# Kernel tuning notes

Measured on AMD Instinct MI355X. Metric: run time of the kernel, lower is better.

## Reference

```python
import jax, jax.numpy as jnp
import numpy as np

L = 4          # num layers
NH = 128       # hidden channels per layer
FC = 16        # frame_channel = patch^2 * C
HP = 32        # H / patch
WP = 32        # W / patch
K = 5          # filter_size
B = 8
T_PREV = 10
T_AFTER = 10
T_TOTAL = T_PREV + T_AFTER - 1  # 19 generated frames
FORGET_BIAS = 1.0


def _conv(x, w):
    # x: [B, Cin, H, W], w: [Cout, Cin, kh, kw], stride 1, SAME padding
    return jax.lax.conv_general_dilated(
        x, w, (1, 1), 'SAME', dimension_numbers=('NCHW', 'OIHW', 'NCHW'))


def _st_lstm_cell(x, h, c, m, Wx, Wh, Wm, Wo, Wl):
    # Standard PredRNN SpatioTemporalLSTMCell (bias-free convs, no layer norm)
    xc = _conv(x, Wx)   # [B, 7*NH, H, W]
    hc = _conv(h, Wh)   # [B, 4*NH, H, W]
    mc = _conv(m, Wm)   # [B, 3*NH, H, W]
    i_x, f_x, g_x, i_xp, f_xp, g_xp, o_x = jnp.split(xc, 7, axis=1)
    i_h, f_h, g_h, o_h = jnp.split(hc, 4, axis=1)
    i_m, f_m, g_m = jnp.split(mc, 3, axis=1)

    i_t = jax.nn.sigmoid(i_x + i_h)
    f_t = jax.nn.sigmoid(f_x + f_h + FORGET_BIAS)
    g_t = jnp.tanh(g_x + g_h)
    c_new = f_t * c + i_t * g_t

    i_tp = jax.nn.sigmoid(i_xp + i_m)
    f_tp = jax.nn.sigmoid(f_xp + f_m + FORGET_BIAS)
    g_tp = jnp.tanh(g_xp + g_m)
    m_new = f_tp * m + i_tp * g_tp

    mem = jnp.concatenate([c_new, m_new], axis=1)  # [B, 2*NH, H, W]
    o_t = jax.nn.sigmoid(o_x + o_h + _conv(mem, Wo))
    h_new = o_t * jnp.tanh(_conv(mem, Wl))
    return h_new, c_new, m_new


def setup_inputs() -> dict:
    key = jax.random.key(0)
    ks = jax.random.split(key, 9)
    s = jnp.float32(0.02)  # small init scale to keep gates in a sane range
    return {
        'frames_tensor': jax.random.normal(ks[0], (B, T_PREV + T_AFTER, HP, WP, FC), jnp.float32),
        'mask_true': jax.random.uniform(ks[1], (B, T_AFTER - 1, HP, WP, FC), jnp.float32),
        'Wx0': jax.random.normal(ks[2], (7 * NH, FC, K, K), jnp.float32) * s,
        'Wx': jax.random.normal(ks[3], (L - 1, 7 * NH, NH, K, K), jnp.float32) * s,
        'Wh': jax.random.normal(ks[4], (L, 4 * NH, NH, K, K), jnp.float32) * s,
        'Wm': jax.random.normal(ks[5], (L, 3 * NH, NH, K, K), jnp.float32) * s,
        'Wo': jax.random.normal(ks[6], (L, NH, 2 * NH, K, K), jnp.float32) * s,
        'Wl': jax.random.normal(ks[7], (L, NH, 2 * NH, 1, 1), jnp.float32) * s,
        'Wout': jax.random.normal(ks[8], (FC, NH, 1, 1), jnp.float32) * s,
    }


def reference(frames_tensor, mask_true, Wx0, Wx, Wh, Wm, Wo, Wl, Wout):
    # [B,T,H,W,C] -> [B,T,C,H,W]
    frames = jnp.transpose(frames_tensor, (0, 1, 4, 2, 3))
    mask = jnp.transpose(mask_true, (0, 1, 4, 2, 3))

    # For t < data_previous the input is the ground-truth frame (mask == 1);
    # afterwards it is blended with the previous generation x_gen.
    ones = jnp.ones((B, T_PREV, FC, HP, WP), frames.dtype)
    mask_seq = jnp.concatenate([ones, mask], axis=1)  # [B, T_TOTAL, C, H, W]

    frames_t = jnp.transpose(frames[:, :T_TOTAL], (1, 0, 2, 3, 4))  # [T,B,C,H,W]
    mask_t = jnp.transpose(mask_seq, (1, 0, 2, 3, 4))               # [T,B,C,H,W]

    h0 = jnp.zeros((L, B, NH, HP, WP), frames.dtype)
    c0 = jnp.zeros((L, B, NH, HP, WP), frames.dtype)
    m0 = jnp.zeros((B, NH, HP, WP), frames.dtype)
    xg0 = jnp.zeros((B, FC, HP, WP), frames.dtype)

    def step(carry, xs):
        h, c, m, x_gen = carry
        frame, msk = xs
        net = msk * frame + (1.0 - msk) * x_gen
        h_new, c_new, m = _st_lstm_cell(net, h[0], c[0], m, Wx0, Wh[0], Wm[0], Wo[0], Wl[0])
        hs, cs = [h_new], [c_new]
        for i in range(1, L):
            hi, ci, m = _st_lstm_cell(hs[-1], h[i], c[i], m, Wx[i - 1], Wh[i], Wm[i], Wo[i], Wl[i])
            hs.append(hi)
            cs.append(ci)
        x_gen = _conv(hs[-1], Wout)  # 1x1 conv, no bias
        return (jnp.stack(hs), jnp.stack(cs), m, x_gen), x_gen

    _, next_frames = jax.lax.scan(step, (h0, c0, m0, xg0), (frames_t, mask_t))
    # [T,B,C,H,W] -> [B,T,H,W,C]
    return jnp.transpose(next_frames, (1, 0, 3, 4, 2))
```

## Files before the change

kernel.cpp:

```cpp
#include <hip/hip_runtime.h>
#include <math.h>

#define TT 19
#define TPREV 10

typedef __attribute__((ext_vector_type(8))) short bf8v;
typedef __attribute__((ext_vector_type(4))) float f4v;
typedef __attribute__((ext_vector_type(16))) float f16v;

__device__ __forceinline__ float sigmoidf_(float x){ return 1.f/(1.f+expf(-x)); }
__device__ __forceinline__ unsigned short f2bf(float x){
    unsigned int u = __float_as_uint(x);
    u += 0x7FFFu + ((u>>16)&1u);
    return (unsigned short)(u>>16);
}
__device__ __forceinline__ float bf2f(unsigned short b){ return __uint_as_float(((unsigned int)b)<<16); }

#define GLDS(g, l) __builtin_amdgcn_global_load_lds( \
    (const __attribute__((address_space(1))) void*)(g),   \
    (__attribute__((address_space(3))) void*)(l), 16, 0, 0)

struct HSeg {
    const unsigned short* in;
    int cl;
    int c0;
    int nch;
    int tap0, ntaps, five;
};
struct HJob {
    const unsigned short* wt;
    float* out;
    int cout_stride, pad;
    HSeg s;
};
struct HJobs14 { HJob j[14]; };
struct HJobs9  { HJob j[9]; };

__device__ __forceinline__ void stage_halo(
    unsigned short* sH, const unsigned short* inb, int cl, int c0,
    int y0, int tid)
{
#pragma unroll
    for (int k = 0; k < 8; ++k) {
        const int s = tid + k * 256;
        if (s < 1920) {
            const int r = s / 160;
            const int rem = s - r * 160;
            const int cc = rem >> 2, G = rem & 3;
            const int y = y0 + r - 2, x = cc - 4;
            const bool okv = ((unsigned)y < 32u) & ((unsigned)x < 32u);
            const int yc = okv ? y : 0, xc = okv ? x : 0;
            bf8v v = *(const bf8v*)(inb + ((((yc << 5) + xc)) << cl) + c0 + G * 8);
            if (!okv) v = (bf8v)(short)0;
            *(bf8v*)&sH[(G * 480 + r * 40 + cc) * 8] = v;
        }
    }
}

template<typename JOBS>
__global__ __launch_bounds__(256, 2) void hconvA_kernel(JOBS jobs)
{
    __shared__ unsigned short sA[16384];
    __shared__ unsigned short sH[15360];
    const int tid = threadIdx.x;

    const int nb   = gridDim.x * gridDim.y;
    const int per8 = nb >> 3;
    const int bidl = blockIdx.x + gridDim.x * blockIdx.y;
    const int g    = (bidl & 7) * per8 + (bidl >> 3);
    const int jy   = g >> 5;
    const int xt   = g & 31;
    const HJob jb = jobs.j[jy];

    const int ng0 = xt << 8;
    const int bb = ng0 >> 10, p0 = ng0 & 1023;
    const int y0 = p0 >> 5;

    const int lane = tid & 63, wv = tid >> 6;
    const int wm = (wv & 1) << 6;
    const int wn = (wv >> 1) << 7;
    const int col = lane & 31, ll5 = lane >> 5;

    int bofs0[4];
#pragma unroll
    for (int ni = 0; ni < 4; ++ni) {
        const int ln = wn + ni * 32 + col;
        const int cell = ((ln >> 5) + 2) * 40 + (ln & 31) + 4;
        bofs0[ni] = cell * 8 + ll5 * 3840;
    }
    const int rowA0 = (wm + col) * 8;
    const int oA = ll5 * 1024;

    f16v acc[2][4];
#pragma unroll
    for (int i = 0; i < 2; ++i)
#pragma unroll
        for (int j = 0; j < 4; ++j) acc[i][j] = (f16v)0.f;

    const HSeg sg = jb.s;
    const unsigned short* inb = sg.in + ((size_t)bb << (10 + sg.cl));
    const unsigned short* wissue = jb.wt;
    const int nch = sg.nch;

    stage_halo(sH, inb, sg.cl, sg.c0, y0, tid);
    GLDS(wissue + tid * 8,                &sA[tid * 8]);
    GLDS(wissue + (tid + 256) * 8,        &sA[(tid + 256) * 8]);
    GLDS(wissue + 4096 + tid * 8,         &sA[4096 + tid * 8]);
    GLDS(wissue + 4096 + (tid + 256) * 8, &sA[4096 + (tid + 256) * 8]);
    wissue += 8192;

    int gg = 0;
    for (int c = 0; c < nch; ++c) {
        if (c > 0) {
            __syncthreads();
            stage_halo(sH, inb, sg.cl, sg.c0 + c * 32, y0, tid);
        }
        const bool last = (c == nch - 1);
        for (int j = 0; j < 13; ++j, ++gg) {
            asm volatile("s_waitcnt vmcnt(0) lgkmcnt(0)" ::: "memory");
            __builtin_amdgcn_s_barrier();
            __builtin_amdgcn_sched_barrier(0);
            const int nIss = (j == 11) ? 1 : ((j == 12) ? (last ? 0 : 2) : 2);
            const int sb1 = ((gg + 1) & 1) << 1;
            for (int q = 0; q < nIss; ++q) {
                GLDS(wissue + tid * 8,         &sA[(sb1 + q) * 4096 + tid * 8]);
                GLDS(wissue + (tid + 256) * 8, &sA[(sb1 + q) * 4096 + (tid + 256) * 8]);
                wissue += 4096;
            }
            const int sb0 = (gg & 1) << 1;
            const int k0 = j << 1;
            const bool pair = (j < 12);
            int t5 = (k0 * 52) >> 8;
            const int tOa = ((t5 - 2) * 40 + (k0 - t5 * 5 - 2)) * 8;
            const unsigned short* sA0 = &sA[sb0 * 4096];
            bf8v av0[2][2], bv0[2][4], av1[2][2], bv1[2][4];
#pragma unroll
            for (int s = 0; s < 2; ++s) {
#pragma unroll
                for (int mi = 0; mi < 2; ++mi)
                    av0[s][mi] = *(const bf8v*)&sA0[s * 2048 + oA + rowA0 + mi * 256];
#pragma unroll
                for (int ni = 0; ni < 4; ++ni)
                    bv0[s][ni] = *(const bf8v*)&sH[bofs0[ni] + tOa + s * 7680];
            }
            if (pair) {
                const int k1 = k0 + 1;
                t5 = (k1 * 52) >> 8;
                const int tOb = ((t5 - 2) * 40 + (k1 - t5 * 5 - 2)) * 8;
                const unsigned short* sA1 = &sA[(sb0 + 1) * 4096];
#pragma unroll
                for (int s = 0; s < 2; ++s) {
#pragma unroll
                    for (int mi = 0; mi < 2; ++mi)
                        av1[s][mi] = *(const bf8v*)&sA1[s * 2048 + oA + rowA0 + mi * 256];
#pragma unroll
                    for (int ni = 0; ni < 4; ++ni)
                        bv1[s][ni] = *(const bf8v*)&sH[bofs0[ni] + tOb + s * 7680];
                }
            }
            __builtin_amdgcn_s_setprio(1);
#pragma unroll
            for (int s = 0; s < 2; ++s)
#pragma unroll
                for (int mi = 0; mi < 2; ++mi)
#pragma unroll
                    for (int ni = 0; ni < 4; ++ni)
                        acc[mi][ni] = __builtin_amdgcn_mfma_f32_32x32x16_bf16(
                            av0[s][mi], bv0[s][ni], acc[mi][ni], 0, 0, 0);
            if (pair) {
#pragma unroll
                for (int s = 0; s < 2; ++s)
#pragma unroll
                    for (int mi = 0; mi < 2; ++mi)
#pragma unroll
                        for (int ni = 0; ni < 4; ++ni)
                            acc[mi][ni] = __builtin_amdgcn_mfma_f32_32x32x16_bf16(
                                av1[s][mi], bv1[s][ni], acc[mi][ni], 0, 0, 0);
            }
            __builtin_amdgcn_s_setprio(0);
        }
    }

    const int nfix = ng0 + wn + col;
#pragma unroll
    for (int ni = 0; ni < 4; ++ni) {
        const int n = nfix + ni * 32;
        float* ob = jb.out + (size_t)n * jb.cout_stride;
#pragma unroll
        for (int mi = 0; mi < 2; ++mi) {
            const int mb = wm + mi * 32 + 4 * ll5;
            const f16v a = acc[mi][ni];
#pragma unroll
            for (int qd = 0; qd < 4; ++qd) {
                f4v v;
                v[0] = a[qd * 4 + 0]; v[1] = a[qd * 4 + 1];
                v[2] = a[qd * 4 + 2]; v[3] = a[qd * 4 + 3];
                *(f4v*)(ob + mb + qd * 8) = v;
            }
        }
    }
}

template<typename JOBS>
__global__ __launch_bounds__(256) void hconv_kernel(JOBS jobs)
{
    __shared__ unsigned short sA[8192];
    __shared__ unsigned short sH[10240];
    const HJob jb = jobs.j[blockIdx.y];
    const int tid = threadIdx.x;

    const int ng0 = blockIdx.x * 128;
    const int bb = ng0 >> 10, p0 = ng0 & 1023;
    const int y0 = p0 >> 5;

    const int lane = tid & 63, wv = tid >> 6;
    const int wm = (wv & 1) << 6;
    const int wn = (wv >> 1) << 6;
    const int col = lane & 31, ll5 = lane >> 5;

    int bofs0[2];
#pragma unroll
    for (int ni = 0; ni < 2; ++ni) {
        const int ln = wn + ni * 32 + col;
        const int cell = ((ln >> 5) + 2) * 40 + (ln & 31) + 4;
        bofs0[ni] = cell * 8 + ll5 * 2560;
    }

    f16v acc[2][2];
#pragma unroll
    for (int i = 0; i < 2; ++i)
#pragma unroll
        for (int j = 0; j < 2; ++j) acc[i][j] = (f16v)0.f;

    const HSeg sg = jb.s;
    const unsigned short* inb = sg.in + ((size_t)bb << (10 + sg.cl));
    const unsigned short* wptr = jb.wt;
    int buf = 0;
    bool first = true;
    for (int ch = 0; ch < sg.nch; ++ch) {
        const int c0 = sg.c0 + ch * 32;
#pragma unroll
        for (int k = 0; k < 5; ++k) {
            const int s = tid + k * 256;
            const int r = s / 160;
            const int rem = s - r * 160;
            const int cc = rem >> 2, G = rem & 3;
            const int y = y0 + r - 2, x = cc - 4;
            const bool okv = ((unsigned)y < 32u) & ((unsigned)x < 32u);
            const int yc = okv ? y : 0, xc = okv ? x : 0;
            bf8v v = *(const bf8v*)(inb + ((((yc << 5) + xc)) << sg.cl) + c0 + G * 8);
            if (!okv) v = (bf8v)(short)0;
            *(bf8v*)&sH[(G * 320 + r * 40 + cc) * 8] = v;
        }
        if (first) {
            GLDS(wptr + tid * 8,         &sA[tid * 8]);
            GLDS(wptr + (tid + 256) * 8, &sA[(tid + 256) * 8]);
            wptr += 4096;
            first = false;
        }
        __syncthreads();
        for (int t = 0; t < sg.ntaps; ++t) {
            GLDS(wptr + tid * 8,         &sA[(buf ^ 1) * 4096 + tid * 8]);
            GLDS(wptr + (tid + 256) * 8, &sA[(buf ^ 1) * 4096 + (tid + 256) * 8]);
            wptr += 4096;
            int tO = 0;
            if (sg.five) {
                const int tap = sg.tap0 + t;
                const int t5 = (tap * 52) >> 8;
                tO = ((t5 - 2) * 40 + (tap - t5 * 5 - 2)) * 8;
            }
            const unsigned short* sAb = &sA[buf * 4096];
#pragma unroll
            for (int s = 0; s < 2; ++s) {
                const int o = s * 2 + ll5;
                bf8v av[2], bv[2];
#pragma unroll
                for (int mi = 0; mi < 2; ++mi)
                    av[mi] = *(const bf8v*)&sAb[(o * 128 + wm + mi * 32 + col) * 8];
#pragma unroll
                for (int ni = 0; ni < 2; ++ni)
                    bv[ni] = *(const bf8v*)&sH[bofs0[ni] + tO + s * 5120];
#pragma unroll
                for (int mi = 0; mi < 2; ++mi)
#pragma unroll
                    for (int ni = 0; ni < 2; ++ni)
                        acc[mi][ni] = __builtin_amdgcn_mfma_f32_32x32x16_bf16(
                            av[mi], bv[ni], acc[mi][ni], 0, 0, 0);
            }
            __syncthreads();
            buf ^= 1;
        }
    }

    const int nfix = ng0 + wn + col;
#pragma unroll
    for (int ni = 0; ni < 2; ++ni) {
        const int n = nfix + ni * 32;
        float* ob = jb.out + (size_t)n * jb.cout_stride;
#pragma unroll
        for (int mi = 0; mi < 2; ++mi) {
            const int mb = wm + mi * 32 + 4 * ll5;
            const f16v a = acc[mi][ni];
#pragma unroll
            for (int qd = 0; qd < 4; ++qd) {
                f4v v;
                v[0] = a[qd * 4 + 0]; v[1] = a[qd * 4 + 1];
                v[2] = a[qd * 4 + 2]; v[3] = a[qd * 4 + 3];
                *(f4v*)(ob + mb + qd * 8) = v;
            }
        }
    }
}

__global__ __launch_bounds__(256) void packT_kernel(
    const float* __restrict__ src, unsigned short* __restrict__ dst,
    int Cin, int srcTaps, int rowOff, int ci0, int ntaps, int tap0,
    int ciMax, int total)
{
    const int idx = blockIdx.x * 256 + threadIdx.x;
    if (idx >= total) return;
    const int j = idx & 7;
    const int row = (idx >> 3) & 127;
    const int q = (idx >> 10) & 3;
    const int at = idx >> 12;
    const int ch = at / ntaps;
    const int tap = tap0 + (at - ch * ntaps);
    const int ci = ci0 + ch * 32 + q * 8 + j;
    float v = 0.f;
    if (ci < ciMax)
        v = src[((size_t)(rowOff + row) * Cin + ci) * srcTaps + tap];
    dst[idx] = f2bf(v);
}

__global__ __launch_bounds__(256) void net_kernel(
    const float* __restrict__ frames, const float* __restrict__ mask,
    const float* __restrict__ xgen, unsigned short* __restrict__ net, int t)
{
    const int idx = blockIdx.x * 256 + threadIdx.x;
    const int n = idx >> 5, ch = idx & 31;
    float v = 0.f;
    if (ch < 16) {
        const int b = n >> 10, p = n & 1023;
        const float fr = frames[((((size_t)b * 20 + t) << 10) + p) * 16 + ch];
        if (t < TPREV) v = fr;
        else {
            const float mk = mask[((((size_t)b * 9 + (t - TPREV)) << 10) + p) * 16 + ch];
            v = mk * fr + (1.f - mk) * xgen[(size_t)n * 16 + ch];
        }
    }
    net[idx] = f2bf(v);
}

__global__ __launch_bounds__(256) void gates_kernel(
    const float* __restrict__ preA, const float* __restrict__ preB,
    float* __restrict__ c, float* __restrict__ m,
    unsigned short* __restrict__ m_bf, unsigned short* __restrict__ mem)
{
    const int idx = blockIdx.x * 256 + threadIdx.x;
    const int n = idx >> 7, ch = idx & 127;
    const float* pa = preA + (size_t)n * 896 + ch;
    const float* pb = preB + (size_t)n * 896 + ch;
    const float i_ = pa[0]   + pb[0];
    const float f_ = pa[128] + pb[128];
    const float g_ = pa[256] + pb[256];
    const float ip = pa[384] + pb[384];
    const float fp = pa[512] + pb[512];
    const float gp = pa[640] + pb[640];
    const float cn = sigmoidf_(f_ + 1.f) * c[idx] + sigmoidf_(i_) * tanhf(g_);
    const float mn = sigmoidf_(fp + 1.f) * m[idx] + sigmoidf_(ip) * tanhf(gp);
    c[idx] = cn;
    m[idx] = mn;
    m_bf[idx] = f2bf(mn);
    mem[(size_t)n * 256 + ch] = f2bf(cn);
    mem[(size_t)n * 256 + 128 + ch] = f2bf(mn);
}

__global__ __launch_bounds__(256) void hout_kernel(
    const float* __restrict__ preA, const float* __restrict__ preB,
    const float* __restrict__ opart, const float* __restrict__ lconv,
    unsigned short* __restrict__ h)
{
    const int idx = blockIdx.x * 256 + threadIdx.x;
    const int n = idx >> 7, ch = idx & 127;
    float oc = preA[(size_t)n * 896 + 768 + ch] + preB[(size_t)n * 896 + 768 + ch];
#pragma unroll
    for (int j = 0; j < 8; ++j) oc += opart[idx + (size_t)j * 1048576];
    h[idx] = f2bf(sigmoidf_(oc) * tanhf(lconv[idx]));
}

__global__ __launch_bounds__(256) void wout_kernel(
    const unsigned short* __restrict__ h3, const float* __restrict__ wo,
    float* __restrict__ xgen, float* __restrict__ out, int t)
{
    const int idx = blockIdx.x * 256 + threadIdx.x;
    const int n = idx >> 4, ch = idx & 15;
    const int b = n >> 10, p = n & 1023;
    const unsigned short* hr = h3 + (size_t)n * 128;
    const float* wr = wo + ch * 128;
    float acc = 0.f;
#pragma unroll 8
    for (int ci = 0; ci < 128; ++ci)
        acc = fmaf(bf2f(hr[ci]), wr[ci], acc);
    xgen[idx] = acc;
    out[((((size_t)b * TT + t) << 10) + p) * 16 + ch] = acc;
}

extern "C" void kernel_launch(void* const* d_in, const int* in_sizes, int n_in,
                              void* d_out, int out_size, void* d_ws, size_t ws_size,
                              hipStream_t stream)
{
    const float* frames = (const float*)d_in[0];
    const float* mask   = (const float*)d_in[1];
    const float* Wx0    = (const float*)d_in[2];
    const float* Wx     = (const float*)d_in[3];
    const float* Wh     = (const float*)d_in[4];
    const float* Wm     = (const float*)d_in[5];
    const float* Wo     = (const float*)d_in[6];
    const float* Wl     = (const float*)d_in[7];
    const float* Wout   = (const float*)d_in[8];
    float* out = (float*)d_out;

    char* base = (char*)d_ws;
    size_t off = 0;
    auto take = [&](size_t bytes) -> char* {
        char* p = base + off;
        off = (off + bytes + 255) & ~(size_t)255;
        return p;
    };
    float* c0            = (float*)take(4ull * 1048576 * 4);
    float* m32           = (float*)take((size_t)1048576 * 4);
    unsigned short* hbf  = (unsigned short*)take(4ull * 1048576 * 2);
    unsigned short* mbf  = (unsigned short*)take((size_t)1048576 * 2);
    const size_t zbytes = off;
    float* xgen          = (float*)take((size_t)131072 * 4);
    float* preA          = (float*)take((size_t)8192 * 896 * 4);
    float* preB          = (float*)take((size_t)8192 * 896 * 4);
    float* lconv         = (float*)take((size_t)1048576 * 4);
    float* opart         = (float*)take(8ull * 1048576 * 4);
    unsigned short* net  = (unsigned short*)take((size_t)262144 * 2);
    unsigned short* mem  = (unsigned short*)take((size_t)2097152 * 2);
    unsigned short* pa0xT = (unsigned short*)take(((size_t)7 * 25 * 4096 + 4096) * 2);
    unsigned short* paT0 = (unsigned short*)take(((size_t)7 * 100 * 4096 + 4096) * 2);
    unsigned short* paT1 = (unsigned short*)take(((size_t)7 * 200 * 4096 + 4096) * 2);
    unsigned short* paT2 = (unsigned short*)take(((size_t)7 * 200 * 4096 + 4096) * 2);
    unsigned short* paT3 = (unsigned short*)take(((size_t)7 * 200 * 4096 + 4096) * 2);
    unsigned short* paT[4] = { paT0, paT1, paT2, paT3 };
    unsigned short* oT   = (unsigned short*)take((4ull * 200 * 4096 + 4096) * 2);
    unsigned short* lT   = (unsigned short*)take((4ull * 8 * 4096 + 4096) * 2);

    hipMemsetAsync(d_ws, 0, zbytes, stream);

    auto packT = [&](const float* s, unsigned short* d, int Cin, int srcTaps,
                     int rowOff, int ci0, int nch, int ntaps, int tap0, int ciMax) {
        const int total = nch * ntaps * 4096;
        packT_kernel<<<(total + 255) / 256, 256, 0, stream>>>(
            s, d, Cin, srcTaps, rowOff, ci0, ntaps, tap0, ciMax, total);
    };
    const int CIMAXBIG = 1 << 30;
    for (int g = 0; g < 7; ++g) {
        packT(Wx0, pa0xT + (size_t)g * 25 * 4096, 16, 25, g * 128, 0, 1, 25, 0, 16);
        const float* hm0 = (g < 3) ? (Wh + (size_t)g * 128 * 128 * 25)
                         : (g == 6) ? (Wh + (size_t)384 * 128 * 25)
                                    : (Wm + (size_t)(g - 3) * 128 * 128 * 25);
        packT(hm0, paT0 + (size_t)g * 100 * 4096, 128, 25, 0, 0, 4, 25, 0, CIMAXBIG);
        for (int l = 1; l < 4; ++l) {
            packT(Wx + (size_t)(l - 1) * 896 * 128 * 25,
                  paT[l] + (size_t)g * 200 * 4096, 128, 25, g * 128, 0, 4, 25, 0, CIMAXBIG);
            const float* hmsrc = (g < 3) ? (Wh + ((size_t)l * 512 + g * 128) * 128 * 25)
                               : (g == 6) ? (Wh + ((size_t)l * 512 + 384) * 128 * 25)
                                          : (Wm + ((size_t)l * 384 + (g - 3) * 128) * 128 * 25);
            packT(hmsrc, paT[l] + ((size_t)g * 200 + 100) * 4096, 128, 25, 0, 0, 4, 25, 0, CIMAXBIG);
        }
    }
    for (int l = 0; l < 4; ++l) {
        packT(Wo + (size_t)l * 128 * 256 * 25, oT + (size_t)l * 200 * 4096,
              256, 25, 0, 0, 8, 25, 0, CIMAXBIG);
        packT(Wl + (size_t)l * 128 * 256, lT + (size_t)l * 8 * 4096,
              256, 1, 0, 0, 8, 1, 0, CIMAXBIG);
    }

    for (int t = 0; t < TT; ++t) {
        net_kernel<<<1024, 256, 0, stream>>>(frames, mask, xgen, net, t);
        for (int l = 0; l < 4; ++l) {
            unsigned short* hl = hbf + (size_t)l * 1048576;
            HJobs14 JA{};
            if (l == 0) {
                for (int g = 0; g < 7; ++g) {
                    const unsigned short* hmsrc = (g < 3 || g == 6) ? hl : mbf;
                    JA.j[2 * g] = HJob{ pa0xT + (size_t)g * 25 * 4096, preA + g * 128,
                                        896, 0, HSeg{ net, 5, 0, 1, 0, 25, 1 } };
                    JA.j[2 * g + 1] = HJob{ paT0 + (size_t)g * 100 * 4096, preB + g * 128,
                                            896, 0, HSeg{ hmsrc, 7, 0, 4, 0, 25, 1 } };
                }
            } else {
                for (int g = 0; g < 7; ++g) {
                    const unsigned short* hmsrc = (g < 3 || g == 6) ? hl : mbf;
                    JA.j[g] = HJob{ paT[l] + (size_t)g * 200 * 4096, preA + g * 128,
                                    896, 0, HSeg{ hbf + (size_t)(l - 1) * 1048576, 7, 0, 4, 0, 25, 1 } };
                    JA.j[7 + g] = HJob{ paT[l] + ((size_t)g * 200 + 100) * 4096, preB + g * 128,
                                        896, 0, HSeg{ hmsrc, 7, 0, 4, 0, 25, 1 } };
                }
            }
            hconvA_kernel<HJobs14><<<dim3(32, 14), 256, 0, stream>>>(JA);

            gates_kernel<<<4096, 256, 0, stream>>>(preA, preB,
                c0 + (size_t)l * 1048576, m32, mbf, mem);

            HJobs9 JB{};
            for (int jj = 0; jj < 8; ++jj)
                JB.j[jj] = HJob{ oT + ((size_t)l * 200 + jj * 25) * 4096,
                                 opart + (size_t)jj * 1048576, 128, 0,
                                 HSeg{ mem, 8, jj * 32, 1, 0, 25, 1 } };
            JB.j[8] = HJob{ lT + (size_t)l * 8 * 4096, lconv, 128, 0,
                            HSeg{ mem, 8, 0, 8, 0, 1, 0 } };
            hconv_kernel<HJobs9><<<dim3(64, 9), 256, 0, stream>>>(JB);

            hout_kernel<<<4096, 256, 0, stream>>>(preA, preB, opart, lconv, hl);
        }
        wout_kernel<<<512, 256, 0, stream>>>(hbf + (size_t)3 * 1048576, Wout, xgen, out, t);
    }
}
```

Measured before the change: 11.01 ms.

## Restructure conv GEMM main loop into 4-slot weight ring with finer-grained waits

Replaces the two-tap-per-iteration double-buffered weight staging with a 4-slot ring buffer in LDS. Each tap gets its own barrier and a partial vmcnt wait, so up to two taps of weights are in flight while the current tap computes. The halo reads for the next tap are software-pipelined ahead of the current MFMA block. The goal is to hide global-to-LDS weight latency and cut full vmcnt(0) stalls, at the cost of twice as many barriers and an extra sync after halo staging.

```diff
diff --git a/kernel.cpp b/kernel.cpp
--- a/kernel.cpp
+++ b/kernel.cpp
@@ -101,83 +101,82 @@
     const unsigned short* inb = sg.in + ((size_t)bb << (10 + sg.cl));
     const unsigned short* wissue = jb.wt;
     const int nch = sg.nch;
+    const int ntot = nch * 25;
+
+    bf8v av[2][2], bvA[2][4], bvB[2][4];
+
+    auto issue = [&](int gt1) {
+        const int sl = (gt1 & 3) * 4096;
+        GLDS(wissue + tid * 8,         &sA[sl + tid * 8]);
+        GLDS(wissue + (tid + 256) * 8, &sA[sl + (tid + 256) * 8]);
+        wissue += 4096;
+    };
+    auto rdA = [&](int slot) {
+        const unsigned short* sAb = &sA[slot * 4096];
+#pragma unroll
+        for (int s = 0; s < 2; ++s)
+#pragma unroll
+            for (int mi = 0; mi < 2; ++mi)
+                av[s][mi] = *(const bf8v*)&sAb[s * 2048 + oA + rowA0 + mi * 256];
+    };
+    auto rdB = [&](bf8v (&bv)[2][4], int kk) {
+        const int t5 = (kk * 52) >> 8;
+        const int tO = ((t5 - 2) * 40 + (kk - t5 * 5 - 2)) * 8;
+#pragma unroll
+        for (int s = 0; s < 2; ++s)
+#pragma unroll
+            for (int ni = 0; ni < 4; ++ni)
+                bv[s][ni] = *(const bf8v*)&sH[bofs0[ni] + tO + s * 7680];
+    };
+    auto mm = [&](bf8v (&bv)[2][4]) {
+        __builtin_amdgcn_s_setprio(1);
+#pragma unroll
+        for (int s = 0; s < 2; ++s)
+#pragma unroll
+            for (int mi = 0; mi < 2; ++mi)
+#pragma unroll
+                for (int ni = 0; ni < 4; ++ni)
+                    acc[mi][ni] = __builtin_amdgcn_mfma_f32_32x32x16_bf16(
+                        av[s][mi], bv[s][ni], acc[mi][ni], 0, 0, 0);
+        __builtin_amdgcn_s_setprio(0);
+    };
 
     stage_halo(sH, inb, sg.cl, sg.c0, y0, tid);
-    GLDS(wissue + tid * 8,                &sA[tid * 8]);
-    GLDS(wissue + (tid + 256) * 8,        &sA[(tid + 256) * 8]);
-    GLDS(wissue + 4096 + tid * 8,         &sA[4096 + tid * 8]);
-    GLDS(wissue + 4096 + (tid + 256) * 8, &sA[4096 + (tid + 256) * 8]);
-    wissue += 8192;
-
-    int gg = 0;
+    issue(0);
+    issue(1);
+    asm volatile("s_waitcnt vmcnt(2) lgkmcnt(0)" ::: "memory");
+    __builtin_amdgcn_s_barrier();
+
     for (int c = 0; c < nch; ++c) {
+        const int gt0 = c * 25;
         if (c > 0) {
             __syncthreads();
             stage_halo(sH, inb, sg.cl, sg.c0 + c * 32, y0, tid);
-        }
-        const bool last = (c == nch - 1);
-        for (int j = 0; j < 13; ++j, ++gg) {
-            asm volatile("s_waitcnt vmcnt(0) lgkmcnt(0)" ::: "memory");
+            __syncthreads();
+        }
+        rdB(bvA, 0);
+        for (int jj = 0; jj < 12; ++jj) {
+            const int ta = gt0 + 2 * jj;
+            if (ta + 2 < ntot) { issue(ta + 2); asm volatile("s_waitcnt vmcnt(2)" ::: "memory"); }
+            else               {                asm volatile("s_waitcnt vmcnt(0)" ::: "memory"); }
             __builtin_amdgcn_s_barrier();
-            __builtin_amdgcn_sched_barrier(0);
-            const int nIss = (j == 11) ? 1 : ((j == 12) ? (last ? 0 : 2) : 2);
-            const int sb1 = ((gg + 1) & 1) << 1;
-            for (int q = 0; q < nIss; ++q) {
-                GLDS(wissue + tid * 8,         &sA[(sb1 + q) * 4096 + tid * 8]);
-                GLDS(wissue + (tid + 256) * 8, &sA[(sb1 + q) * 4096 + (tid + 256) * 8]);
-                wissue += 4096;
-            }
-            const int sb0 = (gg & 1) << 1;
-            const int k0 = j << 1;
-            const bool pair = (j < 12);
-            int t5 = (k0 * 52) >> 8;
-            const int tOa = ((t5 - 2) * 40 + (k0 - t5 * 5 - 2)) * 8;
-            const unsigned short* sA0 = &sA[sb0 * 4096];
-            bf8v av0[2][2], bv0[2][4], av1[2][2], bv1[2][4];
-#pragma unroll
-            for (int s = 0; s < 2; ++s) {
-#pragma unroll
-                for (int mi = 0; mi < 2; ++mi)
-                    av0[s][mi] = *(const bf8v*)&sA0[s * 2048 + oA + rowA0 + mi * 256];
-#pragma unroll
-                for (int ni = 0; ni < 4; ++ni)
-                    bv0[s][ni] = *(const bf8v*)&sH[bofs0[ni] + tOa + s * 7680];
-            }
-            if (pair) {
-                const int k1 = k0 + 1;
-                t5 = (k1 * 52) >> 8;
-                const int tOb = ((t5 - 2) * 40 + (k1 - t5 * 5 - 2)) * 8;
-                const unsigned short* sA1 = &sA[(sb0 + 1) * 4096];
-#pragma unroll
-                for (int s = 0; s < 2; ++s) {
-#pragma unroll
-                    for (int mi = 0; mi < 2; ++mi)
-                        av1[s][mi] = *(const bf8v*)&sA1[s * 2048 + oA + rowA0 + mi * 256];
-#pragma unroll
-                    for (int ni = 0; ni < 4; ++ni)
-                        bv1[s][ni] = *(const bf8v*)&sH[bofs0[ni] + tOb + s * 7680];
-                }
-            }
-            __builtin_amdgcn_s_setprio(1);
-#pragma unroll
-            for (int s = 0; s < 2; ++s)
-#pragma unroll
-                for (int mi = 0; mi < 2; ++mi)
-#pragma unroll
-                    for (int ni = 0; ni < 4; ++ni)
-                        acc[mi][ni] = __builtin_amdgcn_mfma_f32_32x32x16_bf16(
-                            av0[s][mi], bv0[s][ni], acc[mi][ni], 0, 0, 0);
-            if (pair) {
-#pragma unroll
-                for (int s = 0; s < 2; ++s)
-#pragma unroll
-                    for (int mi = 0; mi < 2; ++mi)
-#pragma unroll
-                        for (int ni = 0; ni < 4; ++ni)
-                            acc[mi][ni] = __builtin_amdgcn_mfma_f32_32x32x16_bf16(
-                                av1[s][mi], bv1[s][ni], acc[mi][ni], 0, 0, 0);
-            }
-            __builtin_amdgcn_s_setprio(0);
+            rdA(ta & 3);
+            rdB(bvB, 2 * jj + 1);
+            mm(bvA);
+            if (ta + 3 < ntot) { issue(ta + 3); asm volatile("s_waitcnt vmcnt(2)" ::: "memory"); }
+            else               {                asm volatile("s_waitcnt vmcnt(0)" ::: "memory"); }
+            __builtin_amdgcn_s_barrier();
+            rdA((ta + 1) & 3);
+            rdB(bvA, 2 * jj + 2);
+            mm(bvB);
+        }
+        {
+            const int ta = gt0 + 24;
+            if (ta + 2 < ntot) { issue(ta + 2); asm volatile("s_waitcnt vmcnt(2)" ::: "memory"); }
+            else               {                asm volatile("s_waitcnt vmcnt(0)" ::: "memory"); }
+            __builtin_amdgcn_s_barrier();
+            rdA(ta & 3);
+            mm(bvA);
         }
     }
 
```

Measured after the change: 10.89 ms. Within noise of the previous version (-1.1%).
